# Kernel optimization log

Hardware: AMD Instinct MI355X
Metric: run time of the kernel (lower is better)

The kernel has to match this reference:

```python
import jax, jax.numpy as jnp
import numpy as np

D_MODEL = 256
D_INNER = 512   # expand=2
D_STATE = 16
D_CONV = 4
DT_RANK = 16    # ceil(256/16)
N_LAYERS = 4
BATCH = 16
SEQLEN = 1024


def setup_inputs() -> dict:
    key = jax.random.key(0)
    ks = jax.random.split(key, 30)
    rn = lambda k, shape, s=0.02: (jax.random.normal(k, shape, jnp.float32) * s)
    # packet features: proto in [0,255], len, flags in [0,63], iat, dir in {0,1}
    u = jax.random.uniform(ks[0], (BATCH, SEQLEN, 5), jnp.float32)
    x = u * jnp.array([255.0, 1.0, 63.0, 1.0, 1.0], jnp.float32)
    L = N_LAYERS
    inp = {
        'x': x,
        # PacketEmbedder
        'emb_proto': rn(ks[1], (256, 32)),
        'emb_flags': rn(ks[2], (64, 32)),
        'emb_dir': rn(ks[3], (2, 8)),
        'proj_len_w': rn(ks[4], (32, 1)), 'proj_len_b': rn(ks[5], (32,)),
        'proj_iat_w': rn(ks[6], (32, 1)), 'proj_iat_b': rn(ks[7], (32,)),
        'fusion_w': rn(ks[8], (D_MODEL, 136)), 'fusion_b': rn(ks[9], (D_MODEL,)),
        'tok_norm_g': jnp.ones((D_MODEL,)), 'tok_norm_b': jnp.zeros((D_MODEL,)),
        # shared post-block LayerNorm
        'norm_g': jnp.ones((D_MODEL,)), 'norm_b': jnp.zeros((D_MODEL,)),
        # 4 Mamba blocks, params stacked on leading layer dim
        'in_proj_w': rn(ks[10], (L, 2 * D_INNER, D_MODEL)),
        'conv_w': rn(ks[11], (L, D_INNER, D_CONV), 0.1),
        'conv_b': rn(ks[12], (L, D_INNER)),
        'x_proj_w': rn(ks[13], (L, DT_RANK + 2 * D_STATE, D_INNER)),
        'dt_w': rn(ks[14], (L, D_INNER, DT_RANK)),
        'dt_b': rn(ks[15], (L, D_INNER)),
        'A_log': jnp.log(jnp.tile(jnp.arange(1, D_STATE + 1, dtype=jnp.float32)[None, None, :], (L, D_INNER, 1))),
        'D_param': jnp.ones((L, D_INNER)),
        'out_proj_w': rn(ks[16], (L, D_MODEL, D_INNER)),
        # exit classifier '32' (eval mode, dropout = identity)
        'cls_w1': rn(ks[17], (128, D_MODEL)), 'cls_b1': rn(ks[18], (128,)),
        'cls_w2': rn(ks[19], (2, 128)), 'cls_b2': rn(ks[20], (2,)),
    }
    return inp


def _ln(h, g, b):
    m = h.mean(-1, keepdims=True)
    v = ((h - m) ** 2).mean(-1, keepdims=True)
    return (h - m) / jnp.sqrt(v + 1e-5) * g + b


def _mamba(u, ipw, cw, cb, xpw, dtw, dtb, alog, dprm, opw):
    # u: [B, L, D_MODEL]
    xz = u @ ipw.T                                   # [B, L, 2*Di]
    xx, z = jnp.split(xz, 2, axis=-1)
    # causal depthwise conv1d over time
    xt = xx.transpose(0, 2, 1)                       # [B, Di, L]
    xc = jax.lax.conv_general_dilated(
        xt, cw[:, None, :], (1,), [(D_CONV - 1, 0)],
        dimension_numbers=('NCH', 'OIH', 'NCH'), feature_group_count=D_INNER)
    xc = jax.nn.silu(xc + cb[None, :, None]).transpose(0, 2, 1)  # [B, L, Di]
    dbl = xc @ xpw.T                                 # [B, L, dt_rank + 2*N]
    dtr = dbl[..., :DT_RANK]
    Bm = dbl[..., DT_RANK:DT_RANK + D_STATE]         # [B, L, N]
    Cm = dbl[..., DT_RANK + D_STATE:]                # [B, L, N]
    dt = jax.nn.softplus(dtr @ dtw.T + dtb)          # [B, L, Di]
    A = -jnp.exp(alog)                               # [Di, N]

    def step(h, inp):
        dt_t, B_t, C_t, x_t = inp                    # [B,Di],[B,N],[B,N],[B,Di]
        dA = jnp.exp(dt_t[:, :, None] * A)           # [B, Di, N]
        h = dA * h + (dt_t * x_t)[:, :, None] * B_t[:, None, :]
        return h, jnp.einsum('bdn,bn->bd', h, C_t)

    h0 = jnp.zeros((u.shape[0], D_INNER, D_STATE), u.dtype)
    xs = (dt.transpose(1, 0, 2), Bm.transpose(1, 0, 2),
          Cm.transpose(1, 0, 2), xc.transpose(1, 0, 2))
    _, ys = jax.lax.scan(step, h0, xs)               # ys: [L, B, Di]
    y = ys.transpose(1, 0, 2) + dprm * xc
    y = y * jax.nn.silu(z)
    return y @ opw.T                                 # [B, L, D_MODEL]


def reference(x, emb_proto, emb_flags, emb_dir, proj_len_w, proj_len_b,
              proj_iat_w, proj_iat_b, fusion_w, fusion_b, tok_norm_g, tok_norm_b,
              norm_g, norm_b, in_proj_w, conv_w, conv_b, x_proj_w, dt_w, dt_b,
              A_log, D_param, out_proj_w, cls_w1, cls_b1, cls_w2, cls_b2):
    proto = jnp.clip(x[:, :, 0].astype(jnp.int32), 0, 255)
    length = x[:, :, 1:2]
    flags = jnp.clip(x[:, :, 2].astype(jnp.int32), 0, 63)
    iat = x[:, :, 3:4]
    direc = jnp.clip(x[:, :, 4].astype(jnp.int32), 0, 1)
    cat = jnp.concatenate([
        emb_proto[proto],
        length @ proj_len_w.T + proj_len_b,
        emb_flags[flags],
        iat @ proj_iat_w.T + proj_iat_b,
        emb_dir[direc],
    ], axis=-1)                                      # [B, L, 136]
    feat = _ln(cat @ fusion_w.T + fusion_b, tok_norm_g, tok_norm_b)
    for i in range(N_LAYERS):
        y = _mamba(feat, in_proj_w[i], conv_w[i], conv_b[i], x_proj_w[i],
                   dt_w[i], dt_b[i], A_log[i], D_param[i], out_proj_w[i])
        feat = _ln(y + feat, norm_g, norm_b)
    idx = min(32, feat.shape[1]) - 1
    h = feat[:, idx, :]
    h = jax.nn.relu(h @ cls_w1.T + cls_b1)
    return h @ cls_w2.T + cls_b2                     # [B, 2]
```

## Files before the change

kernel.cpp:

```cpp
#include <hip/hip_runtime.h>
#include <cmath>

#define TT 32
#define NTOK 512
#define DM 256
#define DI 512

typedef float vf4 __attribute__((ext_vector_type(4)));

__device__ __forceinline__ float silu_(float x){ return x / (1.f + __expf(-x)); }

#define FMA16() do { \
  acc[0][0] += xv.x*wv.x; acc[0][1] += xv.x*wv.y; acc[0][2] += xv.x*wv.z; acc[0][3] += xv.x*wv.w; \
  acc[1][0] += xv.y*wv.x; acc[1][1] += xv.y*wv.y; acc[1][2] += xv.y*wv.z; acc[1][3] += xv.y*wv.w; \
  acc[2][0] += xv.z*wv.x; acc[2][1] += xv.z*wv.y; acc[2][2] += xv.z*wv.z; acc[2][3] += xv.z*wv.w; \
  acc[3][0] += xv.w*wv.x; acc[3][1] += xv.w*wv.y; acc[3][2] += xv.w*wv.z; acc[3][3] += xv.w*wv.w; \
} while(0)

__global__ __launch_bounds__(128)
void k_front(const float* __restrict__ x,
             const float* __restrict__ ep, const float* __restrict__ ef,
             const float* __restrict__ ed,
             const float* __restrict__ plw, const float* __restrict__ plb,
             const float* __restrict__ piw, const float* __restrict__ pib,
             const float* __restrict__ fw,  const float* __restrict__ fb,
             float* __restrict__ s0)
{
  __shared__ float Xs[136*36];
  __shared__ float Ws[136*68];
  int bb = blockIdx.x;
  int n0 = blockIdx.y*64;
  int tid = threadIdx.x;
  for (int r = 0; r < 34; ++r){
    int idx = r*128 + tid;
    int t = idx & 31, j = idx >> 5;
    const float* xr = x + ((size_t)(bb*1024 + t))*5;
    float v;
    if      (j <  32){ int i = __float2int_rz(xr[0]); i = min(max(i,0),255); v = ep[i*32 + j]; }
    else if (j <  64){ v = xr[1]*plw[j-32] + plb[j-32]; }
    else if (j <  96){ int i = __float2int_rz(xr[2]); i = min(max(i,0),63);  v = ef[i*32 + (j-64)]; }
    else if (j < 128){ v = xr[3]*piw[j-96] + pib[j-96]; }
    else             { int i = __float2int_rz(xr[4]); i = min(max(i,0),1);   v = ed[i*8 + (j-128)]; }
    Xs[j*36 + t] = v;
  }
  {
    int c = tid >> 1, jh = tid & 1;
    const float4* src = (const float4*)(fw + (size_t)(n0 + c)*136 + jh*68);
    #pragma unroll
    for (int q = 0; q < 17; ++q){
      float4 v = src[q];
      int j = jh*68 + q*4;
      Ws[(j+0)*68 + c] = v.x; Ws[(j+1)*68 + c] = v.y;
      Ws[(j+2)*68 + c] = v.z; Ws[(j+3)*68 + c] = v.w;
    }
  }
  __syncthreads();
  int my = tid >> 4, nx = tid & 15;
  float acc[4][4] = {};
  #pragma unroll 4
  for (int k = 0; k < 136; ++k){
    float4 xv = *(const float4*)&Xs[k*36 + my*4];
    float4 wv = *(const float4*)&Ws[k*68 + nx*4];
    FMA16();
  }
  #pragma unroll
  for (int i = 0; i < 4; ++i){
    int t = my*4 + i;
    float4 o;
    o.x = acc[i][0] + fb[n0 + nx*4 + 0];
    o.y = acc[i][1] + fb[n0 + nx*4 + 1];
    o.z = acc[i][2] + fb[n0 + nx*4 + 2];
    o.w = acc[i][3] + fb[n0 + nx*4 + 3];
    *(float4*)&s0[(size_t)(bb*32 + t)*DM + n0 + nx*4] = o;
  }
}

__global__ __launch_bounds__(512)
void k_A(const float* __restrict__ wip, const float* __restrict__ cwl,
         const float* __restrict__ cbl, const float* __restrict__ xpl,
         const float* __restrict__ g, const float* __restrict__ bb,
         const float* __restrict__ parts, int resid,
         const float* __restrict__ featIn, float* __restrict__ featOut,
         float* __restrict__ xc, float* __restrict__ zs, float* __restrict__ pxp)
{
  extern __shared__ float lds[];
  float* featT = lds;
  float* Ws    = lds + 9216;
  float* sxz   = lds + 13568;
  float* xcl   = lds + 15648;
  int tid = threadIdx.x;
  int b = blockIdx.x, nt = blockIdx.y;
  int n0 = nt*64;

  {
    int t = tid & 31, ci = tid >> 5;
    size_t base = (size_t)(b*32 + t)*DM + ci*16;
    float v[16];
    {
      const float4* p0 = (const float4*)(parts + base);
      #pragma unroll
      for (int q = 0; q < 4; ++q){
        float4 u = p0[q];
        v[q*4+0]=u.x; v[q*4+1]=u.y; v[q*4+2]=u.z; v[q*4+3]=u.w;
      }
    }
    if (resid){
      #pragma unroll
      for (int p2 = 1; p2 < 8; ++p2){
        const float4* pq = (const float4*)(parts + (size_t)p2*NTOK*DM + base);
        #pragma unroll
        for (int q = 0; q < 4; ++q){
          float4 u = pq[q];
          v[q*4+0]+=u.x; v[q*4+1]+=u.y; v[q*4+2]+=u.z; v[q*4+3]+=u.w;
        }
      }
      const float4* pf = (const float4*)(featIn + base);
      #pragma unroll
      for (int q = 0; q < 4; ++q){
        float4 u = pf[q];
        v[q*4+0]+=u.x; v[q*4+1]+=u.y; v[q*4+2]+=u.z; v[q*4+3]+=u.w;
      }
    }
    float s = 0.f, sq = 0.f;
    #pragma unroll
    for (int j = 0; j < 16; ++j){ s += v[j]; sq += v[j]*v[j]; }
    float* redS = Ws; float* redQ = Ws + 544;
    redS[t*17 + ci] = s; redQ[t*17 + ci] = sq;
    __syncthreads();
    float S = 0.f, Q = 0.f;
    #pragma unroll
    for (int k2 = 0; k2 < 16; ++k2){ S += redS[t*17+k2]; Q += redQ[t*17+k2]; }
    float mu = S*(1.f/256.f), var = Q*(1.f/256.f) - mu*mu;
    float r = rsqrtf(var + 1e-5f);
    #pragma unroll
    for (int j = 0; j < 16; ++j){
      int c = ci*16 + j;
      v[j] = (v[j]-mu)*r*g[c] + bb[c];
      featT[c*36 + t] = v[j];
    }
    if (nt == 0){
      #pragma unroll
      for (int q = 0; q < 4; ++q){
        float4 o = {v[q*4+0], v[q*4+1], v[q*4+2], v[q*4+3]};
        *(float4*)&featOut[base + q*4] = o;
      }
    }
  }

  int tg = tid >> 6, cc = tid & 63;
  float a0 = 0.f, a1 = 0.f, a2 = 0.f, a3 = 0.f;
  for (int kc = 0; kc < 4; ++kc){
    __syncthreads();
    {
      int c = tid >> 3, kh = tid & 7;
      const float4* src = (const float4*)(wip + (size_t)(n0+c)*DM + kc*64 + kh*8);
      #pragma unroll
      for (int q = 0; q < 2; ++q){
        float4 u = src[q];
        int k = kh*8 + q*4;
        Ws[(k+0)*68 + c] = u.x; Ws[(k+1)*68 + c] = u.y;
        Ws[(k+2)*68 + c] = u.z; Ws[(k+3)*68 + c] = u.w;
      }
    }
    __syncthreads();
    #pragma unroll 8
    for (int kk = 0; kk < 64; ++kk){
      vf4 xv = *(const vf4*)&featT[(kc*64 + kk)*36 + tg*4];
      float wv = Ws[kk*68 + cc];
      a0 += xv[0]*wv; a1 += xv[1]*wv; a2 += xv[2]*wv; a3 += xv[3]*wv;
    }
  }
  __syncthreads();
  sxz[(tg*4+0)*65 + cc] = a0;
  sxz[(tg*4+1)*65 + cc] = a1;
  sxz[(tg*4+2)*65 + cc] = a2;
  sxz[(tg*4+3)*65 + cc] = a3;
  __syncthreads();

  {
    int t = tid >> 4, c4 = (tid & 15)*4;
    float rr[4];
    if (n0 < 512){
      #pragma unroll
      for (int j = 0; j < 4; ++j){
        int c = c4 + j, d = n0 + c;
        float4 k4 = *(const float4*)(cwl + (size_t)d*4);
        float a = cbl[d];
        if (t >= 3) a += k4.x*sxz[(t-3)*65 + c];
        if (t >= 2) a += k4.y*sxz[(t-2)*65 + c];
        if (t >= 1) a += k4.z*sxz[(t-1)*65 + c];
        a += k4.w*sxz[t*65 + c];
        rr[j] = silu_(a);
        xcl[t*65 + c] = rr[j];
      }
      float4 o = {rr[0], rr[1], rr[2], rr[3]};
      *(float4*)&xc[(size_t)(b*32 + t)*DI + n0 + c4] = o;
    } else {
      #pragma unroll
      for (int j = 0; j < 4; ++j) rr[j] = silu_(sxz[t*65 + c4 + j]);
      float4 o = {rr[0], rr[1], rr[2], rr[3]};
      *(float4*)&zs[(size_t)(b*32 + t)*DI + (n0 - 512) + c4] = o;
    }
  }
  if (n0 < 512){
    __syncthreads();
    int w = tid >> 6, ln = tid & 63;
    int tt = ln & 31, half = ln >> 5;
    #pragma unroll
    for (int j = 0; j < 6; ++j){
      int c = w*6 + j;
      const float* wr = xpl + (size_t)c*DI + n0 + half*32;
      const float* xr = xcl + tt*65 + half*32;
      float pa = 0.f;
      #pragma unroll 8
      for (int q = 0; q < 32; ++q) pa += wr[q]*xr[q];
      pa += __shfl_xor(pa, 32, 64);
      if (half == 0) pxp[((size_t)(b*8 + nt)*48 + c)*32 + tt] = pa;
    }
  }
}

__global__ __launch_bounds__(512)
void k_sc(const float* __restrict__ pxp,
          const float* __restrict__ dtwl, const float* __restrict__ dtbl,
          const float* __restrict__ alogl, const float* __restrict__ dprl,
          const float* __restrict__ opwl,
          const float* __restrict__ xc, const float* __restrict__ zs,
          float* __restrict__ parts)
{
  __shared__ float sdtr[32*18], sB[32*18], sC[32*18];
  __shared__ float sdt[32*68], sxv[32*68], szz[32*68];
  __shared__ float ygT[64*36];
  __shared__ float Wop[32*260];
  int tid = threadIdx.x;
  int b = blockIdx.x, ds = blockIdx.y;
  int d0 = ds*64;

  #pragma unroll
  for (int r = 0; r < 3; ++r){
    int o = r*512 + tid;
    int c = o >> 5, t = o & 31;
    size_t p0 = ((size_t)(b*8)*48 + c)*32 + t;
    float v = 0.f;
    #pragma unroll
    for (int nb = 0; nb < 8; ++nb) v += pxp[p0 + (size_t)nb*1536];
    if      (c < 16) sdtr[t*18 + c] = v;
    else if (c < 32) sB[t*18 + (c-16)] = v;
    else             sC[t*18 + (c-32)] = v;
  }
  {
    int t = tid >> 4, dq = (tid & 15)*4;
    size_t base = (size_t)(b*32 + t)*DI + d0 + dq;
    *(float4*)&sxv[t*68 + dq] = *(const float4*)&xc[base];
    *(float4*)&szz[t*68 + dq] = *(const float4*)&zs[base];
  }
  __syncthreads();
  {
    int dl = tid & 63, tg2 = tid >> 6;
    int d = d0 + dl;
    const float4* dwr = (const float4*)(dtwl + (size_t)d*16);
    float4 w0 = dwr[0], w1 = dwr[1], w2 = dwr[2], w3 = dwr[3];
    float bsv = dtbl[d];
    #pragma unroll
    for (int tt2 = 0; tt2 < 4; ++tt2){
      int t = tg2*4 + tt2;
      const float* sr = &sdtr[t*18];
      float a = bsv;
      a += w0.x*sr[0] + w0.y*sr[1] + w0.z*sr[2] + w0.w*sr[3];
      a += w1.x*sr[4] + w1.y*sr[5] + w1.z*sr[6] + w1.w*sr[7];
      a += w2.x*sr[8] + w2.y*sr[9] + w2.z*sr[10]+ w2.w*sr[11];
      a += w3.x*sr[12]+ w3.y*sr[13]+ w3.z*sr[14]+ w3.w*sr[15];
      sdt[t*68 + dl] = fmaxf(a, 0.f) + log1pf(expf(-fabsf(a)));
    }
  }
  __syncthreads();
  {
    int dd = tid >> 3, ng = tid & 7;
    int d = d0 + dd;
    int n0i = ng*2;
    float A0 = -expf(alogl[(size_t)d*16 + n0i]);
    float A1 = -expf(alogl[(size_t)d*16 + n0i + 1]);
    float Dp = dprl[d];
    float h0 = 0.f, h1 = 0.f;
    #pragma unroll 4
    for (int t = 0; t < TT; ++t){
      float dt = sdt[t*68 + dd];
      float xv = sxv[t*68 + dd];
      float dx = dt*xv;
      h0 = __expf(dt*A0)*h0 + dx*sB[t*18 + n0i];
      h1 = __expf(dt*A1)*h1 + dx*sB[t*18 + n0i + 1];
      float yv = h0*sC[t*18 + n0i] + h1*sC[t*18 + n0i + 1];
      yv += __shfl_xor(yv, 1, 64);
      yv += __shfl_xor(yv, 2, 64);
      yv += __shfl_xor(yv, 4, 64);
      if (ng == 0) ygT[dd*36 + t] = (yv + Dp*xv) * szz[t*68 + dd];
    }
  }
  int cW = tid >> 1, khW = tid & 1;
  int w = tid >> 6, cq = (tid & 63)*4;
  float acc[4][4] = {};
  for (int kc = 0; kc < 2; ++kc){
    __syncthreads();
    {
      const float4* src = (const float4*)(opwl + (size_t)cW*DI + d0 + kc*32 + khW*16);
      #pragma unroll
      for (int q = 0; q < 4; ++q){
        float4 u = src[q];
        int k = khW*16 + q*4;
        Wop[(k+0)*260 + cW] = u.x; Wop[(k+1)*260 + cW] = u.y;
        Wop[(k+2)*260 + cW] = u.z; Wop[(k+3)*260 + cW] = u.w;
      }
    }
    __syncthreads();
    #pragma unroll 4
    for (int k = 0; k < 32; ++k){
      vf4 xv = *(const vf4*)&ygT[(kc*32 + k)*36 + w*4];
      vf4 wv = *(const vf4*)&Wop[k*260 + cq];
      #pragma unroll
      for (int i = 0; i < 4; ++i){
        #pragma unroll
        for (int j = 0; j < 4; ++j) acc[i][j] += xv[i]*wv[j];
      }
    }
  }
  float* dst = parts + (size_t)ds*NTOK*DM;
  #pragma unroll
  for (int i = 0; i < 4; ++i){
    float4 o = {acc[i][0], acc[i][1], acc[i][2], acc[i][3]};
    *(float4*)&dst[(size_t)(b*32 + w*4 + i)*DM + cq] = o;
  }
}

__global__ __launch_bounds__(128)
void k_cls(const float* __restrict__ feat3, const float* __restrict__ parts,
           const float* __restrict__ ng, const float* __restrict__ nb,
           const float* __restrict__ w1, const float* __restrict__ b1,
           const float* __restrict__ w2, const float* __restrict__ b2,
           float* __restrict__ out)
{
  __shared__ float h[256];
  __shared__ float h1[128];
  int b = blockIdx.x, tid = threadIdx.x;
  if (tid < 64){
    int c4 = tid*4;
    size_t base = (size_t)(b*32 + 31)*DM + c4;
    float4 v = *(const float4*)&feat3[base];
    #pragma unroll
    for (int q = 0; q < 8; ++q){
      float4 u = *(const float4*)&parts[(size_t)q*NTOK*DM + base];
      v.x += u.x; v.y += u.y; v.z += u.z; v.w += u.w;
    }
    float sm = v.x+v.y+v.z+v.w;
    float sq = v.x*v.x+v.y*v.y+v.z*v.z+v.w*v.w;
    #pragma unroll
    for (int o = 1; o < 64; o <<= 1){ sm += __shfl_xor(sm, o, 64); sq += __shfl_xor(sq, o, 64); }
    float mu = sm*(1.f/256.f), var = sq*(1.f/256.f) - mu*mu;
    float r = rsqrtf(var + 1e-5f);
    h[c4+0] = (v.x-mu)*r*ng[c4+0] + nb[c4+0];
    h[c4+1] = (v.y-mu)*r*ng[c4+1] + nb[c4+1];
    h[c4+2] = (v.z-mu)*r*ng[c4+2] + nb[c4+2];
    h[c4+3] = (v.w-mu)*r*ng[c4+3] + nb[c4+3];
  }
  __syncthreads();
  {
    float a = b1[tid];
    const float* wr = w1 + (size_t)tid*256;
    #pragma unroll 8
    for (int j = 0; j < 256; ++j) a += h[j]*wr[j];
    h1[tid] = fmaxf(a, 0.f);
  }
  __syncthreads();
  if (tid < 2){
    float a2 = b2[tid];
    const float* wr2 = w2 + (size_t)tid*128;
    #pragma unroll 8
    for (int j = 0; j < 128; ++j) a2 += h1[j]*wr2[j];
    out[b*2 + tid] = a2;
  }
}

extern "C" void kernel_launch(void* const* d_in, const int* in_sizes, int n_in,
                              void* d_out, int out_size, void* d_ws, size_t ws_size,
                              hipStream_t stream)
{
  const float* x   = (const float*)d_in[0];
  const float* ep  = (const float*)d_in[1];
  const float* ef  = (const float*)d_in[2];
  const float* ed  = (const float*)d_in[3];
  const float* plw = (const float*)d_in[4];
  const float* plb = (const float*)d_in[5];
  const float* piw = (const float*)d_in[6];
  const float* pib = (const float*)d_in[7];
  const float* fw  = (const float*)d_in[8];
  const float* fb  = (const float*)d_in[9];
  const float* tg  = (const float*)d_in[10];
  const float* tb  = (const float*)d_in[11];
  const float* ng  = (const float*)d_in[12];
  const float* nb  = (const float*)d_in[13];
  const float* ipw = (const float*)d_in[14];
  const float* cw  = (const float*)d_in[15];
  const float* cb  = (const float*)d_in[16];
  const float* xpw = (const float*)d_in[17];
  const float* dtw = (const float*)d_in[18];
  const float* dtb = (const float*)d_in[19];
  const float* alog= (const float*)d_in[20];
  const float* dpr = (const float*)d_in[21];
  const float* opw = (const float*)d_in[22];
  const float* w1  = (const float*)d_in[23];
  const float* b1  = (const float*)d_in[24];
  const float* w2  = (const float*)d_in[25];
  const float* b2  = (const float*)d_in[26];
  (void)in_sizes; (void)n_in; (void)out_size; (void)ws_size;

  float* ws    = (float*)d_ws;
  float* s0    = ws;
  float* fb0   = s0  + NTOK*DM;
  float* fb1   = fb0 + NTOK*DM;
  float* parts = fb1 + NTOK*DM;
  float* pxp   = parts + 8*NTOK*DM;
  float* xc    = pxp + 196608;
  float* zs    = xc  + NTOK*DI;
  float* fbuf[2] = {fb0, fb1};

  k_front<<<dim3(16,4),128,0,stream>>>(x, ep,ef,ed, plw,plb,piw,pib, fw,fb, s0);

  for (int ly = 0; ly < 4; ++ly){
    const float* gg = ly ? ng : tg;
    const float* gb = ly ? nb : tb;
    const float* pin = ly ? parts : s0;
    const float* fin = ly ? fbuf[(ly+1)&1] : nullptr;
    k_A<<<dim3(16,16),512,70912,stream>>>(ipw + (size_t)ly*262144,
                                          cw + (size_t)ly*2048, cb + (size_t)ly*512,
                                          xpw + (size_t)ly*24576,
                                          gg, gb, pin, ly ? 1 : 0, fin,
                                          fbuf[ly&1], xc, zs, pxp);
    k_sc<<<dim3(16,8),512,0,stream>>>(pxp,
                                      dtw + (size_t)ly*8192, dtb + (size_t)ly*512,
                                      alog + (size_t)ly*8192, dpr + (size_t)ly*512,
                                      opw + (size_t)ly*131072,
                                      xc, zs, parts);
  }
  k_cls<<<16,128,0,stream>>>(fbuf[1], parts, ng, nb, w1, b1, w2, b2, (float*)d_out);
}
```

Before: 195.2 us.

## Shrink k_A to 256 threads with a 4x4 register-tiled in_proj GEMM

Halves the k_A block to 256 threads and rewrites the in_proj GEMM as a 4x4 outer-product register tile computed by 128 threads, loading float4 weights and activations from LDS. Each thread now covers twice as much work in the LayerNorm, conv/SiLU and x_proj stages, and the LDS row stride changes to 68 for aligned float4 stores. The goal is more FMAs per LDS load. The cost is that half the threads sit idle during the GEMM and the block has fewer waves to hide latency.

```diff
diff --git a/kernel.cpp b/kernel.cpp
--- a/kernel.cpp
+++ b/kernel.cpp
@@ -75,7 +75,7 @@
   }
 }
 
-__global__ __launch_bounds__(512)
+__global__ __launch_bounds__(256)
 void k_A(const float* __restrict__ wip, const float* __restrict__ cwl,
          const float* __restrict__ cbl, const float* __restrict__ xpl,
          const float* __restrict__ g, const float* __restrict__ bb,
@@ -87,19 +87,19 @@
   float* featT = lds;
   float* Ws    = lds + 9216;
   float* sxz   = lds + 13568;
-  float* xcl   = lds + 15648;
+  float* xcl   = lds + 15744;
   int tid = threadIdx.x;
   int b = blockIdx.x, nt = blockIdx.y;
   int n0 = nt*64;
 
   {
     int t = tid & 31, ci = tid >> 5;
-    size_t base = (size_t)(b*32 + t)*DM + ci*16;
-    float v[16];
+    size_t base = (size_t)(b*32 + t)*DM + ci*32;
+    float v[32];
     {
       const float4* p0 = (const float4*)(parts + base);
       #pragma unroll
-      for (int q = 0; q < 4; ++q){
+      for (int q = 0; q < 8; ++q){
         float4 u = p0[q];
         v[q*4+0]=u.x; v[q*4+1]=u.y; v[q*4+2]=u.z; v[q*4+3]=u.w;
       }
@@ -109,97 +109,106 @@
       for (int p2 = 1; p2 < 8; ++p2){
         const float4* pq = (const float4*)(parts + (size_t)p2*NTOK*DM + base);
         #pragma unroll
-        for (int q = 0; q < 4; ++q){
+        for (int q = 0; q < 8; ++q){
           float4 u = pq[q];
           v[q*4+0]+=u.x; v[q*4+1]+=u.y; v[q*4+2]+=u.z; v[q*4+3]+=u.w;
         }
       }
       const float4* pf = (const float4*)(featIn + base);
       #pragma unroll
-      for (int q = 0; q < 4; ++q){
+      for (int q = 0; q < 8; ++q){
         float4 u = pf[q];
         v[q*4+0]+=u.x; v[q*4+1]+=u.y; v[q*4+2]+=u.z; v[q*4+3]+=u.w;
       }
     }
     float s = 0.f, sq = 0.f;
     #pragma unroll
-    for (int j = 0; j < 16; ++j){ s += v[j]; sq += v[j]*v[j]; }
-    float* redS = Ws; float* redQ = Ws + 544;
-    redS[t*17 + ci] = s; redQ[t*17 + ci] = sq;
+    for (int j = 0; j < 32; ++j){ s += v[j]; sq += v[j]*v[j]; }
+    float* redS = Ws; float* redQ = Ws + 288;
+    redS[t*9 + ci] = s; redQ[t*9 + ci] = sq;
     __syncthreads();
     float S = 0.f, Q = 0.f;
     #pragma unroll
-    for (int k2 = 0; k2 < 16; ++k2){ S += redS[t*17+k2]; Q += redQ[t*17+k2]; }
+    for (int k2 = 0; k2 < 8; ++k2){ S += redS[t*9+k2]; Q += redQ[t*9+k2]; }
     float mu = S*(1.f/256.f), var = Q*(1.f/256.f) - mu*mu;
     float r = rsqrtf(var + 1e-5f);
     #pragma unroll
-    for (int j = 0; j < 16; ++j){
-      int c = ci*16 + j;
+    for (int j = 0; j < 32; ++j){
+      int c = ci*32 + j;
       v[j] = (v[j]-mu)*r*g[c] + bb[c];
       featT[c*36 + t] = v[j];
     }
     if (nt == 0){
       #pragma unroll
-      for (int q = 0; q < 4; ++q){
+      for (int q = 0; q < 8; ++q){
         float4 o = {v[q*4+0], v[q*4+1], v[q*4+2], v[q*4+3]};
         *(float4*)&featOut[base + q*4] = o;
       }
     }
   }
 
-  int tg = tid >> 6, cc = tid & 63;
-  float a0 = 0.f, a1 = 0.f, a2 = 0.f, a3 = 0.f;
+  int my = tid >> 4, nx = tid & 15;
+  float acc[4][4] = {};
   for (int kc = 0; kc < 4; ++kc){
     __syncthreads();
     {
-      int c = tid >> 3, kh = tid & 7;
-      const float4* src = (const float4*)(wip + (size_t)(n0+c)*DM + kc*64 + kh*8);
-      #pragma unroll
-      for (int q = 0; q < 2; ++q){
+      int c = tid >> 2, kq = tid & 3;
+      const float4* src = (const float4*)(wip + (size_t)(n0+c)*DM + kc*64 + kq*16);
+      #pragma unroll
+      for (int q = 0; q < 4; ++q){
         float4 u = src[q];
-        int k = kh*8 + q*4;
+        int k = kq*16 + q*4;
         Ws[(k+0)*68 + c] = u.x; Ws[(k+1)*68 + c] = u.y;
         Ws[(k+2)*68 + c] = u.z; Ws[(k+3)*68 + c] = u.w;
       }
     }
     __syncthreads();
-    #pragma unroll 8
-    for (int kk = 0; kk < 64; ++kk){
-      vf4 xv = *(const vf4*)&featT[(kc*64 + kk)*36 + tg*4];
-      float wv = Ws[kk*68 + cc];
-      a0 += xv[0]*wv; a1 += xv[1]*wv; a2 += xv[2]*wv; a3 += xv[3]*wv;
-    }
-  }
-  __syncthreads();
-  sxz[(tg*4+0)*65 + cc] = a0;
-  sxz[(tg*4+1)*65 + cc] = a1;
-  sxz[(tg*4+2)*65 + cc] = a2;
-  sxz[(tg*4+3)*65 + cc] = a3;
-  __syncthreads();
-
-  {
-    int t = tid >> 4, c4 = (tid & 15)*4;
-    float rr[4];
+    if (tid < 128){
+      #pragma unroll 4
+      for (int kk = 0; kk < 64; ++kk){
+        float4 xv = *(const float4*)&featT[(kc*64 + kk)*36 + my*4];
+        float4 wv = *(const float4*)&Ws[kk*68 + nx*4];
+        FMA16();
+      }
+    }
+  }
+  __syncthreads();
+  if (tid < 128){
+    #pragma unroll
+    for (int i = 0; i < 4; ++i){
+      float4 o = {acc[i][0], acc[i][1], acc[i][2], acc[i][3]};
+      *(float4*)&sxz[(my*4 + i)*68 + nx*4] = o;
+    }
+  }
+  __syncthreads();
+
+  {
+    int t = tid >> 3, c8 = (tid & 7)*8;
+    float rr[8];
     if (n0 < 512){
       #pragma unroll
-      for (int j = 0; j < 4; ++j){
-        int c = c4 + j, d = n0 + c;
+      for (int j = 0; j < 8; ++j){
+        int c = c8 + j, d = n0 + c;
         float4 k4 = *(const float4*)(cwl + (size_t)d*4);
         float a = cbl[d];
-        if (t >= 3) a += k4.x*sxz[(t-3)*65 + c];
-        if (t >= 2) a += k4.y*sxz[(t-2)*65 + c];
-        if (t >= 1) a += k4.z*sxz[(t-1)*65 + c];
-        a += k4.w*sxz[t*65 + c];
+        if (t >= 3) a += k4.x*sxz[(t-3)*68 + c];
+        if (t >= 2) a += k4.y*sxz[(t-2)*68 + c];
+        if (t >= 1) a += k4.z*sxz[(t-1)*68 + c];
+        a += k4.w*sxz[t*68 + c];
         rr[j] = silu_(a);
-        xcl[t*65 + c] = rr[j];
-      }
-      float4 o = {rr[0], rr[1], rr[2], rr[3]};
-      *(float4*)&xc[(size_t)(b*32 + t)*DI + n0 + c4] = o;
+        xcl[t*68 + c] = rr[j];
+      }
+      float4 o0 = {rr[0], rr[1], rr[2], rr[3]};
+      float4 o1 = {rr[4], rr[5], rr[6], rr[7]};
+      *(float4*)&xc[(size_t)(b*32 + t)*DI + n0 + c8]     = o0;
+      *(float4*)&xc[(size_t)(b*32 + t)*DI + n0 + c8 + 4] = o1;
     } else {
       #pragma unroll
-      for (int j = 0; j < 4; ++j) rr[j] = silu_(sxz[t*65 + c4 + j]);
-      float4 o = {rr[0], rr[1], rr[2], rr[3]};
-      *(float4*)&zs[(size_t)(b*32 + t)*DI + (n0 - 512) + c4] = o;
+      for (int j = 0; j < 8; ++j) rr[j] = silu_(sxz[t*68 + c8 + j]);
+      float4 o0 = {rr[0], rr[1], rr[2], rr[3]};
+      float4 o1 = {rr[4], rr[5], rr[6], rr[7]};
+      *(float4*)&zs[(size_t)(b*32 + t)*DI + (n0-512) + c8]     = o0;
+      *(float4*)&zs[(size_t)(b*32 + t)*DI + (n0-512) + c8 + 4] = o1;
     }
   }
   if (n0 < 512){
@@ -207,10 +216,10 @@
     int w = tid >> 6, ln = tid & 63;
     int tt = ln & 31, half = ln >> 5;
     #pragma unroll
-    for (int j = 0; j < 6; ++j){
-      int c = w*6 + j;
+    for (int j = 0; j < 12; ++j){
+      int c = w*12 + j;
       const float* wr = xpl + (size_t)c*DI + n0 + half*32;
-      const float* xr = xcl + tt*65 + half*32;
+      const float* xr = xcl + tt*68 + half*32;
       float pa = 0.f;
       #pragma unroll 8
       for (int q = 0; q < 32; ++q) pa += wr[q]*xr[q];
@@ -429,7 +438,7 @@
     const float* gb = ly ? nb : tb;
     const float* pin = ly ? parts : s0;
     const float* fin = ly ? fbuf[(ly+1)&1] : nullptr;
-    k_A<<<dim3(16,16),512,70912,stream>>>(ipw + (size_t)ly*262144,
+    k_A<<<dim3(16,16),256,71680,stream>>>(ipw + (size_t)ly*262144,
                                           cw + (size_t)ly*2048, cb + (size_t)ly*512,
                                           xpw + (size_t)ly*24576,
                                           gg, gb, pin, ly ? 1 : 0, fin,
```

Result: slower. 232.9 us (+19.3%).
